# Kernel optimization log

Hardware: AMD Instinct MI355X
Metric: run time of the kernel (lower is better)

The kernel has to match this reference:

```python
import jax, jax.numpy as jnp
import numpy as np

N_NODES = 100000
N_EDGES = 3200000
N_GRAPHS = 1024

def _lin(x, W, b):
    return x @ W.T + b

def _gine(x, src, dst, edge_attr, W, b, n_nodes):
    # message = relu(x_j + e); aggregate sum at dst; out = Linear(x + aggr)  (eps=0)
    msg = jax.nn.relu(x[src] + edge_attr)
    aggr = jax.ops.segment_sum(msg, dst, num_segments=n_nodes)
    return _lin(x + aggr, W, b)

def setup_inputs() -> dict:
    key = jax.random.key(0)
    ks = jax.random.split(key, 20)
    D_NODE, D_EDGE, H, OUT = 12, 4, 15, 2
    inp = {
        "x": jax.random.normal(ks[0], (N_NODES, D_NODE), dtype=jnp.float32),
        "edge_index": jax.random.randint(ks[1], (2, N_EDGES), 0, N_NODES, dtype=jnp.int64),
        "edge_attr": jax.random.normal(ks[2], (N_EDGES, D_EDGE), dtype=jnp.float32),
        "batch": jnp.sort(jax.random.randint(ks[3], (N_NODES,), 0, N_GRAPHS, dtype=jnp.int64)),
        # edge converters
        "Wec1": jax.random.normal(ks[4], (D_NODE, D_EDGE), dtype=jnp.float32) * 0.3,
        "bec1": jnp.zeros((D_NODE,), jnp.float32),
        "Wec2": jax.random.normal(ks[5], (H, D_NODE), dtype=jnp.float32) * 0.2,
        "bec2": jnp.zeros((H,), jnp.float32),
        # GINE layer linears
        "Wl0": jax.random.normal(ks[6], (H, D_NODE), dtype=jnp.float32) * 0.2,
        "bl0": jnp.zeros((H,), jnp.float32),
        "Wl1": jax.random.normal(ks[7], (H, H), dtype=jnp.float32) * 0.2,
        "bl1": jnp.zeros((H,), jnp.float32),
        "Wl2": jax.random.normal(ks[8], (H, H), dtype=jnp.float32) * 0.2,
        "bl2": jnp.zeros((H,), jnp.float32),
        # output head
        "Wo1": jax.random.normal(ks[9], (H, H), dtype=jnp.float32) * 0.2,
        "bo1": jnp.zeros((H,), jnp.float32),
        "Wo2": jax.random.normal(ks[10], (OUT, H), dtype=jnp.float32) * 0.2,
        "bo2": jnp.zeros((OUT,), jnp.float32),
    }
    return inp

def reference(x, edge_index, edge_attr, batch,
              Wec1, bec1, Wec2, bec2,
              Wl0, bl0, Wl1, bl1, Wl2, bl2,
              Wo1, bo1, Wo2, bo2):
    src, dst = edge_index[0], edge_index[1]
    n = x.shape[0]
    ea = _lin(edge_attr, Wec1, bec1)                 # [E, 12]
    h = jax.nn.elu(_gine(x, src, dst, ea, Wl0, bl0, n))   # [N, 15]
    ea2 = _lin(ea, Wec2, bec2)                       # [E, 15]
    h = jax.nn.elu(_gine(h, src, dst, ea2, Wl1, bl1, n))
    h = jax.nn.elu(_gine(h, src, dst, ea2, Wl2, bl2, n))
    pooled = jax.ops.segment_sum(h, batch, num_segments=N_GRAPHS)  # [G, 15]
    out = _lin(pooled, Wo1, bo1)
    # dropout(p=0.1) is identity in eval mode
    out = _lin(out, Wo2, bo2)                        # [G, 2]
    return out
```

## Files before the change

kernel.cpp:

```cpp
#include <hip/hip_runtime.h>
#include <hip/hip_fp16.h>
#include <math.h>

#define D_NODE 12
#define HS     16
#define BSH    7
#define BSZ    128
#define CHUNK  8192
#define HALF   4096
#define MAXNB  1024

__device__ __forceinline__ int wave_iscan(int v, int lane) {
#pragma unroll
    for (int d = 1; d < 64; d <<= 1) {
        int u = __shfl_up(v, d, 64);
        if (lane >= d) v += u;
    }
    return v;
}

__device__ __forceinline__ uint2 pack4(float4 a) {
    __half2 lo = __floats2half2_rn(a.x, a.y);
    __half2 hi = __floats2half2_rn(a.z, a.w);
    uint2 r;
    r.x = *reinterpret_cast<unsigned*>(&lo);
    r.y = *reinterpret_cast<unsigned*>(&hi);
    return r;
}

__device__ __forceinline__ float4 unpack4(unsigned ux, unsigned uy) {
    __half2 lo = *reinterpret_cast<__half2*>(&ux);
    __half2 hi = *reinterpret_cast<__half2*>(&uy);
    float2 f0 = __half22float2(lo), f1 = __half22float2(hi);
    return make_float4(f0.x, f0.y, f1.x, f1.y);
}

__global__ __launch_bounds__(256) void k_xcvt(
    const float* __restrict__ x, long long nn, __half* __restrict__ xp)
{
    long long idx = (long long)blockIdx.x * 256 + threadIdx.x;
    if (idx >= nn * HS) return;
    long long n = idx >> 4;
    int l = (int)(idx & 15);
    xp[idx] = __float2half_rn((l < D_NODE) ? x[n * D_NODE + l] : 0.f);
}

__global__ __launch_bounds__(1024) void k_p1(
    const int* __restrict__ ei, long long ne, int NB, int* __restrict__ M)
{
    __shared__ int cnt[MAXNB];
    int t = threadIdx.x;
    for (int k = t; k < NB; k += 1024) cnt[k] = 0;
    __syncthreads();
    long long beg = (long long)blockIdx.x * CHUNK;
    long long end = beg + CHUNK; if (end > ne) end = ne;
    for (long long e = beg + t; e < end; e += 1024)
        atomicAdd(&cnt[ei[ne + e] >> BSH], 1);
    __syncthreads();
    int* row = M + (long long)blockIdx.x * NB;
    for (int k = t; k < NB; k += 1024) row[k] = cnt[k];
}

__global__ __launch_bounds__(256) void k_colscan(
    int* __restrict__ M, int nblk, int NB, int* __restrict__ tot)
{
    __shared__ int wsum[4];
    int k = blockIdx.x;
    int t = threadIdx.x;
    int lane = t & 63, wv = t >> 6;
    int v[4]; int s = 0;
#pragma unroll
    for (int j = 0; j < 4; ++j) {
        int b = t * 4 + j;
        v[j] = (b < nblk) ? M[(long long)b * NB + k] : 0;
        s += v[j];
    }
    int inc = wave_iscan(s, lane);
    if (lane == 63) wsum[wv] = inc;
    __syncthreads();
    int base = inc - s;
#pragma unroll
    for (int j = 0; j < 4; ++j) { if (j < wv) base += wsum[j]; }
#pragma unroll
    for (int j = 0; j < 4; ++j) {
        int b = t * 4 + j;
        if (b < nblk) { M[(long long)b * NB + k] = base; base += v[j]; }
    }
    if (t == 255) tot[k] = base;
}

__global__ __launch_bounds__(1024) void k_bb(
    const int* __restrict__ tot, int NB, int* __restrict__ bb)
{
    __shared__ int wsum[16];
    int t = threadIdx.x;
    int lane = t & 63, wv = t >> 6;
    int c = (t < NB) ? tot[t] : 0;
    int inc = wave_iscan(c, lane);
    if (lane == 63) wsum[wv] = inc;
    __syncthreads();
    if (t < 16) {
        int s2 = wsum[t];
#pragma unroll
        for (int d = 1; d < 16; d <<= 1) {
            int u = __shfl_up(s2, d, 64);
            if (t >= d) s2 += u;
        }
        wsum[t] = s2;
    }
    __syncthreads();
    int base = (wv == 0) ? 0 : wsum[wv - 1];
    int incl = base + inc;
    if (t < NB) bb[t] = incl - c;
    if (t == NB - 1) bb[NB] = incl;
}

__global__ __launch_bounds__(1024) void k_p2(
    const int* __restrict__ ei, long long ne, const float4* __restrict__ attr,
    const int* __restrict__ M, const int* __restrict__ bb, int NB,
    unsigned* __restrict__ sp1, uint2* __restrict__ sattr1)
{
    __shared__ int lcnt[MAXNB];
    __shared__ int excl[MAXNB];
    __shared__ int gb[MAXNB];
    __shared__ int wsum[16];
    __shared__ unsigned sp_st[HALF];
    __shared__ uint2   sat_st[HALF];
    __shared__ int     gd_st[HALF];
    int t = threadIdx.x;
    int lane = t & 63, wv = t >> 6;
    const int* row = M + (long long)blockIdx.x * NB;
    gb[t]   = (t < NB) ? (bb[t] + row[t]) : 0;
    lcnt[t] = 0;
    __syncthreads();
    long long beg = (long long)blockIdx.x * CHUNK;
    long long end = beg + CHUNK; if (end > ne) end = ne;
    int nloc = (int)(end - beg);
    unsigned pk8[8]; uint2 a8[8]; int k8[8], r8[8];
#pragma unroll
    for (int j = 0; j < 8; ++j) {
        long long e = beg + t + (long long)j * 1024;
        if (e < end) {
            int s = ei[e];
            int d = ei[ne + e];
            a8[j] = pack4(attr[e]);
            int k = d >> BSH;
            k8[j] = k;
            pk8[j] = (unsigned)s | ((unsigned)(d & (BSZ - 1)) << 20);
            r8[j] = atomicAdd(&lcnt[k], 1);
        } else k8[j] = -1;
    }
    __syncthreads();
    int c = lcnt[t];
    int inc = wave_iscan(c, lane);
    if (lane == 63) wsum[wv] = inc;
    __syncthreads();
    if (t < 16) {
        int s2 = wsum[t];
#pragma unroll
        for (int d = 1; d < 16; d <<= 1) {
            int u = __shfl_up(s2, d, 64);
            if (t >= d) s2 += u;
        }
        wsum[t] = s2;
    }
    __syncthreads();
    excl[t] = inc - c + ((wv == 0) ? 0 : wsum[wv - 1]);
    __syncthreads();
    int idx8[8];
#pragma unroll
    for (int j = 0; j < 8; ++j)
        idx8[j] = (k8[j] >= 0) ? (excl[k8[j]] + r8[j]) : -1;
#pragma unroll
    for (int q = 0; q < 2; ++q) {
        int lo = q * HALF;
#pragma unroll
        for (int j = 0; j < 8; ++j) {
            int idx = idx8[j] - lo;
            if (idx8[j] >= 0 && idx >= 0 && idx < HALF) {
                sp_st[idx]  = pk8[j];
                sat_st[idx] = a8[j];
                gd_st[idx]  = gb[k8[j]] + r8[j];
            }
        }
        __syncthreads();
        for (int p = t; p < HALF; p += 1024) {
            int gp = lo + p;
            if (gp < nloc) {
                int gd = gd_st[p];
                sp1[gd]    = sp_st[p];
                sattr1[gd] = sat_st[p];
            }
        }
        __syncthreads();
    }
}

__global__ __launch_bounds__(1024) void k_p3(
    const unsigned* __restrict__ sp1, const uint2* __restrict__ sattr1,
    const int* __restrict__ bb, int NB, long long nn,
    unsigned* __restrict__ sp2, uint2* __restrict__ sattr2, int* __restrict__ off)
{
    __shared__ int cnt[BSZ];
    __shared__ int stage[BSZ];
    __shared__ int wsum0;
    int k = blockIdx.x, t = threadIdx.x;
    int lane = t & 63, wv = t >> 6;
    int beg = bb[k], end = bb[k + 1];
    if (t < BSZ) cnt[t] = 0;
    __syncthreads();
    for (int e = beg + t; e < end; e += 1024)
        atomicAdd(&cnt[sp1[e] >> 20], 1);
    __syncthreads();
    if (t < BSZ) {
        int c = cnt[t];
        int inc = wave_iscan(c, lane);
        stage[t] = inc;
        if (lane == 63 && wv == 0) wsum0 = inc;
    }
    __syncthreads();
    if (t < BSZ) {
        int c = cnt[t];
        int incl = stage[t] + ((wv == 1) ? wsum0 : 0);
        int excl = beg + incl - c;
        long long n = (long long)k * BSZ + t;
        if (n < nn) off[n] = excl;
        cnt[t] = excl;
    }
    if (k == NB - 1 && t == 0) off[nn] = end;
    __syncthreads();
    for (int e = beg + t; e < end; e += 1024) {
        unsigned pk = sp1[e];
        int ld = pk >> 20;
        int p = atomicAdd(&cnt[ld], 1);
        sp2[p] = pk & 0xFFFFF;
        sattr2[p] = sattr1[e];
    }
}

__global__ __launch_bounds__(256) void k_layer0(
    const __half* __restrict__ xp, long long nn, const int* __restrict__ off,
    const unsigned* __restrict__ sp2, const uint2* __restrict__ sattr2,
    const float* __restrict__ Wec1, const float* __restrict__ bec1,
    const float* __restrict__ Wl, const float* __restrict__ bl,
    __half* __restrict__ hout)
{
    __shared__ float sW1[64], sb1[16], sWl[16 * 17], sbl[16];
    int t = threadIdx.x;
    if (t < 64)  sW1[t] = (t < 48) ? Wec1[t] : 0.f;
    if (t < 16)  sb1[t] = (t < 12) ? bec1[t] : 0.f;
    { int i = t >> 4, j = t & 15;
      sWl[i * 17 + j] = (i < 15 && j < 12) ? Wl[i * 12 + j] : 0.f; }
    if (t < 16)  sbl[t] = (t < 15) ? bl[t] : 0.f;
    __syncthreads();
    int wv = t >> 6;
    int lane = t & 63;
    int l = lane & 15;
    int slot = lane >> 4;
    long long n = (long long)blockIdx.x * 4 + wv;
    if (n >= nn) return;
    int beg = off[n], end = off[n + 1];
    float w0 = sW1[l*4+0], w1 = sW1[l*4+1], w2 = sW1[l*4+2], w3 = sW1[l*4+3];
    float b1 = sb1[l];
    float xn = __half2float(xp[(n << 4) + l]);
    float acc = 0.f;
#pragma unroll 2
    for (int e0 = beg; e0 < end; e0 += 4) {
        int e = e0 + slot;
        unsigned sp = sp2[e] & 0xFFFFF;
        uint2 at = sattr2[e];
        float4 a = unpack4(at.x, at.y);
        float xs = __half2float(xp[((long long)sp << 4) + l]);
        float ea = b1 + w0 * a.x + w1 * a.y + w2 * a.z + w3 * a.w;
        float m = fmaxf(xs + ea, 0.f);
        acc += (e < end) ? m : 0.f;
    }
    acc += __shfl_xor(acc, 16, 64);
    acc += __shfl_xor(acc, 32, 64);
    float v = xn + acc;
    float r = sbl[l];
#pragma unroll
    for (int j = 0; j < 12; ++j) {
        float vj = __shfl(v, j, 16);
        r += vj * sWl[l * 17 + j];
    }
    float o = r > 0.f ? r : expm1f(r);
    if (slot == 0)
        hout[(n << 4) + l] = __float2half_rn((l < 15) ? o : 0.f);
}

template<bool POOL, bool STORE>
__global__ __launch_bounds__(256) void k_layerK(
    const __half* __restrict__ h, long long nn, const int* __restrict__ off,
    const unsigned* __restrict__ sp2, const uint2* __restrict__ sattr2,
    const float* __restrict__ Wec1, const float* __restrict__ bec1,
    const float* __restrict__ Wec2, const float* __restrict__ bec2,
    const float* __restrict__ Wl, const float* __restrict__ bl,
    __half* __restrict__ hout, const int* __restrict__ batch, float* __restrict__ pooled)
{
    __shared__ float sW12[64], sb12[16], sWl[16 * 17], sbl[16];
    int t = threadIdx.x;
    if (t < 64) {
        int i = t >> 2, kk = t & 3;
        float a = 0.f;
        if (i < 15) {
#pragma unroll
            for (int j = 0; j < 12; ++j) a += Wec2[i*12+j] * Wec1[j*4+kk];
        }
        sW12[t] = a;
    }
    if (t < 16) {
        float a = 0.f;
        if (t < 15) {
            a = bec2[t];
#pragma unroll
            for (int j = 0; j < 12; ++j) a += Wec2[t*12+j] * bec1[j];
        }
        sb12[t] = a;
    }
    { int i = t >> 4, j = t & 15;
      sWl[i * 17 + j] = (i < 15 && j < 15) ? Wl[i * 15 + j] : 0.f; }
    if (t < 16) sbl[t] = (t < 15) ? bl[t] : 0.f;
    __syncthreads();
    int wv = t >> 6;
    int lane = t & 63;
    int l = lane & 15;
    int slot = lane >> 4;
    long long n = (long long)blockIdx.x * 4 + wv;
    if (n >= nn) return;
    int beg = off[n], end = off[n + 1];
    float w0 = sW12[l*4+0], w1 = sW12[l*4+1], w2 = sW12[l*4+2], w3 = sW12[l*4+3];
    float b12 = sb12[l];
    float hn = __half2float(h[(n << 4) + l]);
    float acc = 0.f;
#pragma unroll 2
    for (int e0 = beg; e0 < end; e0 += 4) {
        int e = e0 + slot;
        unsigned sp = sp2[e] & 0xFFFFF;
        uint2 at = sattr2[e];
        float4 a = unpack4(at.x, at.y);
        float hs = __half2float(h[((long long)sp << 4) + l]);
        float e2 = b12 + w0 * a.x + w1 * a.y + w2 * a.z + w3 * a.w;
        float m = fmaxf(hs + e2, 0.f);
        acc += (e < end) ? m : 0.f;
    }
    acc += __shfl_xor(acc, 16, 64);
    acc += __shfl_xor(acc, 32, 64);
    float v = hn + acc;
    float r = sbl[l];
#pragma unroll
    for (int j = 0; j < 15; ++j) {
        float vj = __shfl(v, j, 16);
        r += vj * sWl[l * 17 + j];
    }
    float o = r > 0.f ? r : expm1f(r);
    if (slot == 0) {
        if (STORE) hout[(n << 4) + l] = __float2half_rn((l < 15) ? o : 0.f);
        if (POOL && l < 15) atomicAdd(&pooled[(long long)batch[n] * HS + l], o);
    }
}

__global__ __launch_bounds__(256) void k_head(
    const float* __restrict__ pooled, long long ng,
    const float* __restrict__ Wo1, const float* __restrict__ bo1,
    const float* __restrict__ Wo2, const float* __restrict__ bo2,
    float* __restrict__ out)
{
    long long g = (long long)blockIdx.x * 256 + threadIdx.x;
    if (g >= ng) return;
    float p[15], m[15];
#pragma unroll
    for (int j = 0; j < 15; ++j) p[j] = pooled[g * HS + j];
#pragma unroll
    for (int i = 0; i < 15; ++i) {
        float acc = bo1[i];
#pragma unroll
        for (int j = 0; j < 15; ++j) acc += p[j] * Wo1[i * 15 + j];
        m[i] = acc;
    }
#pragma unroll
    for (int i = 0; i < 2; ++i) {
        float acc = bo2[i];
#pragma unroll
        for (int j = 0; j < 15; ++j) acc += m[j] * Wo2[i * 15 + j];
        out[g * 2 + i] = acc;
    }
}

extern "C" void kernel_launch(void* const* d_in, const int* in_sizes, int n_in,
                              void* d_out, int out_size, void* d_ws, size_t ws_size,
                              hipStream_t stream)
{
    const float* x    = (const float*)d_in[0];
    const int*   ei   = (const int*)d_in[1];
    const float* attr = (const float*)d_in[2];
    const int*   batch= (const int*)d_in[3];
    const float* Wec1 = (const float*)d_in[4];
    const float* bec1 = (const float*)d_in[5];
    const float* Wec2 = (const float*)d_in[6];
    const float* bec2 = (const float*)d_in[7];
    const float* Wl0  = (const float*)d_in[8];
    const float* bl0  = (const float*)d_in[9];
    const float* Wl1  = (const float*)d_in[10];
    const float* bl1  = (const float*)d_in[11];
    const float* Wl2  = (const float*)d_in[12];
    const float* bl2  = (const float*)d_in[13];
    const float* Wo1  = (const float*)d_in[14];
    const float* bo1  = (const float*)d_in[15];
    const float* Wo2  = (const float*)d_in[16];
    const float* bo2  = (const float*)d_in[17];

    const long long nn = in_sizes[0] / D_NODE;
    const long long ne = in_sizes[1] / 2;
    const long long ng = out_size / 2;

    const int NB   = (int)((nn + BSZ - 1) >> BSH);
    const int nblk = (int)((ne + CHUNK - 1) / CHUNK);
    const long long nep = ne + 8;

    char* w = (char*)d_ws;
    uint2*    sattr1 = (uint2*)w;                 w += (size_t)nep * sizeof(uint2);
    unsigned* sp1    = (unsigned*)w;              w += (size_t)nep * sizeof(unsigned);
    uint2*    sattr2 = (uint2*)w;                 w += (size_t)nep * sizeof(uint2);
    unsigned* sp2    = (unsigned*)w;              w += (size_t)nep * sizeof(unsigned);
    int*      M      = (int*)w;                   w += (size_t)nblk * NB * sizeof(int);
    int*      tot    = (int*)w;                   w += (size_t)NB * sizeof(int);
    int*      bb     = (int*)w;                   w += ((size_t)NB + 1) * sizeof(int);
    int*      off    = (int*)w;                   w += ((size_t)nn + 1) * sizeof(int);
    w = (char*)(((uintptr_t)w + 15) & ~(uintptr_t)15);
    __half*   xp     = (__half*)w;                w += (size_t)nn * HS * sizeof(__half);
    __half*   hA     = (__half*)sattr1;
    __half*   hB     = hA + (size_t)nn * HS;
    float*    pooled = (float*)(hB + (size_t)nn * HS);
    float*    out    = (float*)d_out;

    k_xcvt<<<(int)((nn * HS + 255) / 256), 256, 0, stream>>>(x, nn, xp);

    k_p1<<<nblk, 1024, 0, stream>>>(ei, ne, NB, M);
    k_colscan<<<NB, 256, 0, stream>>>(M, nblk, NB, tot);
    k_bb<<<1, 1024, 0, stream>>>(tot, NB, bb);
    k_p2<<<nblk, 1024, 0, stream>>>(ei, ne, (const float4*)attr, M, bb, NB, sp1, sattr1);
    k_p3<<<NB, 1024, 0, stream>>>(sp1, sattr1, bb, NB, nn, sp2, sattr2, off);

    const int lblk = (int)((nn + 3) / 4);
    k_layer0<<<lblk, 256, 0, stream>>>(xp, nn, off, sp2, sattr2, Wec1, bec1, Wl0, bl0, hA);
    k_layerK<false, true><<<lblk, 256, 0, stream>>>(hA, nn, off, sp2, sattr2,
        Wec1, bec1, Wec2, bec2, Wl1, bl1, hB, nullptr, nullptr);
    hipMemsetAsync(pooled, 0, (size_t)ng * HS * sizeof(float), stream);
    k_layerK<true, false><<<lblk, 256, 0, stream>>>(hB, nn, off, sp2, sattr2,
        Wec1, bec1, Wec2, bec2, Wl2, bl2, nullptr, batch, pooled);

    k_head<<<(int)((ng + 255) / 256), 256, 0, stream>>>(pooled, ng, Wo1, bo1, Wo2, bo2, out);
}
```

Measured before the change: 324.8 us.

## Remap GINE layer lanes to process 16 edges per wave with 4-wide feature vectors

Changes the thread mapping in the layer kernels so each lane handles 4 feature channels (8-byte half loads) and a wave covers 16 edges per iteration instead of 4. This raises edge-level parallelism per wave and cuts redundant per-edge index and attribute loads, which were repeated 16 times per edge before. The cost is more registers, a longer shuffle reduction and a reworked matvec via cross-lane shuffles. Padding of the sorted edge arrays grows to 16 and the tail of sp2 is zeroed so out-of-range lanes read a valid row.

Measured after the change: 294.8 us. -9.2%, faster.

```diff
diff --git a/kernel.cpp b/kernel.cpp
--- a/kernel.cpp
+++ b/kernel.cpp
@@ -253,40 +253,61 @@
       sWl[i * 17 + j] = (i < 15 && j < 12) ? Wl[i * 12 + j] : 0.f; }
     if (t < 16)  sbl[t] = (t < 15) ? bl[t] : 0.f;
     __syncthreads();
-    int wv = t >> 6;
-    int lane = t & 63;
-    int l = lane & 15;
-    int slot = lane >> 4;
+    int lane = t & 63, wv = t >> 6;
+    int d4 = lane & 3;
+    int slot = lane >> 2;
     long long n = (long long)blockIdx.x * 4 + wv;
     if (n >= nn) return;
     int beg = off[n], end = off[n + 1];
-    float w0 = sW1[l*4+0], w1 = sW1[l*4+1], w2 = sW1[l*4+2], w3 = sW1[l*4+3];
-    float b1 = sb1[l];
-    float xn = __half2float(xp[(n << 4) + l]);
-    float acc = 0.f;
-#pragma unroll 2
-    for (int e0 = beg; e0 < end; e0 += 4) {
+    float w1r[4][4], b1r[4];
+#pragma unroll
+    for (int j = 0; j < 4; ++j) {
+        b1r[j] = sb1[d4 * 4 + j];
+#pragma unroll
+        for (int k = 0; k < 4; ++k) w1r[j][k] = sW1[(d4 * 4 + j) * 4 + k];
+    }
+    float acc[4] = {0.f, 0.f, 0.f, 0.f};
+    for (int e0 = beg; e0 < end; e0 += 16) {
         int e = e0 + slot;
         unsigned sp = sp2[e] & 0xFFFFF;
         uint2 at = sattr2[e];
         float4 a = unpack4(at.x, at.y);
-        float xs = __half2float(xp[((long long)sp << 4) + l]);
-        float ea = b1 + w0 * a.x + w1 * a.y + w2 * a.z + w3 * a.w;
-        float m = fmaxf(xs + ea, 0.f);
-        acc += (e < end) ? m : 0.f;
-    }
-    acc += __shfl_xor(acc, 16, 64);
-    acc += __shfl_xor(acc, 32, 64);
-    float v = xn + acc;
+        uint2 hv = *reinterpret_cast<const uint2*>(
+            reinterpret_cast<const char*>(xp) + ((size_t)sp << 5) + (d4 << 3));
+        float4 hf = unpack4(hv.x, hv.y);
+        float hvf[4] = {hf.x, hf.y, hf.z, hf.w};
+        bool val = (e < end);
+#pragma unroll
+        for (int j = 0; j < 4; ++j) {
+            float ea = b1r[j] + w1r[j][0]*a.x + w1r[j][1]*a.y + w1r[j][2]*a.z + w1r[j][3]*a.w;
+            float m = fmaxf(hvf[j] + ea, 0.f);
+            acc[j] += val ? m : 0.f;
+        }
+    }
+#pragma unroll
+    for (int j = 0; j < 4; ++j) {
+        acc[j] += __shfl_xor(acc[j], 4, 64);
+        acc[j] += __shfl_xor(acc[j], 8, 64);
+        acc[j] += __shfl_xor(acc[j], 16, 64);
+        acc[j] += __shfl_xor(acc[j], 32, 64);
+    }
+    uint2 hnv = *reinterpret_cast<const uint2*>(
+        reinterpret_cast<const char*>(xp) + ((size_t)n << 5) + (d4 << 3));
+    float4 hnf = unpack4(hnv.x, hnv.y);
+    float v4[4] = {hnf.x + acc[0], hnf.y + acc[1], hnf.z + acc[2], hnf.w + acc[3]};
+    int l = lane & 15;
     float r = sbl[l];
 #pragma unroll
-    for (int j = 0; j < 12; ++j) {
-        float vj = __shfl(v, j, 16);
-        r += vj * sWl[l * 17 + j];
+    for (int a2 = 0; a2 < 4; ++a2) {
+#pragma unroll
+        for (int b2 = 0; b2 < 4; ++b2) {
+            float vv = __shfl(v4[b2], a2, 64);
+            r += vv * sWl[l * 17 + a2 * 4 + b2];
+        }
     }
     float o = r > 0.f ? r : expm1f(r);
-    if (slot == 0)
-        hout[(n << 4) + l] = __float2half_rn((l < 15) ? o : 0.f);
+    if (lane < 16)
+        hout[(n << 4) + lane] = __float2half_rn((lane < 15) ? o : 0.f);
 }
 
 template<bool POOL, bool STORE>
@@ -322,41 +343,62 @@
       sWl[i * 17 + j] = (i < 15 && j < 15) ? Wl[i * 15 + j] : 0.f; }
     if (t < 16) sbl[t] = (t < 15) ? bl[t] : 0.f;
     __syncthreads();
-    int wv = t >> 6;
-    int lane = t & 63;
-    int l = lane & 15;
-    int slot = lane >> 4;
+    int lane = t & 63, wv = t >> 6;
+    int d4 = lane & 3;
+    int slot = lane >> 2;
     long long n = (long long)blockIdx.x * 4 + wv;
     if (n >= nn) return;
     int beg = off[n], end = off[n + 1];
-    float w0 = sW12[l*4+0], w1 = sW12[l*4+1], w2 = sW12[l*4+2], w3 = sW12[l*4+3];
-    float b12 = sb12[l];
-    float hn = __half2float(h[(n << 4) + l]);
-    float acc = 0.f;
-#pragma unroll 2
-    for (int e0 = beg; e0 < end; e0 += 4) {
+    float w12r[4][4], b12r[4];
+#pragma unroll
+    for (int j = 0; j < 4; ++j) {
+        b12r[j] = sb12[d4 * 4 + j];
+#pragma unroll
+        for (int k = 0; k < 4; ++k) w12r[j][k] = sW12[(d4 * 4 + j) * 4 + k];
+    }
+    float acc[4] = {0.f, 0.f, 0.f, 0.f};
+    for (int e0 = beg; e0 < end; e0 += 16) {
         int e = e0 + slot;
         unsigned sp = sp2[e] & 0xFFFFF;
         uint2 at = sattr2[e];
         float4 a = unpack4(at.x, at.y);
-        float hs = __half2float(h[((long long)sp << 4) + l]);
-        float e2 = b12 + w0 * a.x + w1 * a.y + w2 * a.z + w3 * a.w;
-        float m = fmaxf(hs + e2, 0.f);
-        acc += (e < end) ? m : 0.f;
-    }
-    acc += __shfl_xor(acc, 16, 64);
-    acc += __shfl_xor(acc, 32, 64);
-    float v = hn + acc;
+        uint2 hv = *reinterpret_cast<const uint2*>(
+            reinterpret_cast<const char*>(h) + ((size_t)sp << 5) + (d4 << 3));
+        float4 hf = unpack4(hv.x, hv.y);
+        float hvf[4] = {hf.x, hf.y, hf.z, hf.w};
+        bool val = (e < end);
+#pragma unroll
+        for (int j = 0; j < 4; ++j) {
+            float e2 = b12r[j] + w12r[j][0]*a.x + w12r[j][1]*a.y + w12r[j][2]*a.z + w12r[j][3]*a.w;
+            float m = fmaxf(hvf[j] + e2, 0.f);
+            acc[j] += val ? m : 0.f;
+        }
+    }
+#pragma unroll
+    for (int j = 0; j < 4; ++j) {
+        acc[j] += __shfl_xor(acc[j], 4, 64);
+        acc[j] += __shfl_xor(acc[j], 8, 64);
+        acc[j] += __shfl_xor(acc[j], 16, 64);
+        acc[j] += __shfl_xor(acc[j], 32, 64);
+    }
+    uint2 hnv = *reinterpret_cast<const uint2*>(
+        reinterpret_cast<const char*>(h) + ((size_t)n << 5) + (d4 << 3));
+    float4 hnf = unpack4(hnv.x, hnv.y);
+    float v4[4] = {hnf.x + acc[0], hnf.y + acc[1], hnf.z + acc[2], hnf.w + acc[3]};
+    int l = lane & 15;
     float r = sbl[l];
 #pragma unroll
-    for (int j = 0; j < 15; ++j) {
-        float vj = __shfl(v, j, 16);
-        r += vj * sWl[l * 17 + j];
+    for (int a2 = 0; a2 < 4; ++a2) {
+#pragma unroll
+        for (int b2 = 0; b2 < 4; ++b2) {
+            float vv = __shfl(v4[b2], a2, 64);
+            r += vv * sWl[l * 17 + a2 * 4 + b2];
+        }
     }
     float o = r > 0.f ? r : expm1f(r);
-    if (slot == 0) {
-        if (STORE) hout[(n << 4) + l] = __float2half_rn((l < 15) ? o : 0.f);
-        if (POOL && l < 15) atomicAdd(&pooled[(long long)batch[n] * HS + l], o);
+    if (lane < 16) {
+        if (STORE) hout[(n << 4) + lane] = __float2half_rn((lane < 15) ? o : 0.f);
+        if (POOL && lane < 15) atomicAdd(&pooled[(long long)batch[n] * HS + lane], o);
     }
 }
 
@@ -416,7 +458,7 @@
 
     const int NB   = (int)((nn + BSZ - 1) >> BSH);
     const int nblk = (int)((ne + CHUNK - 1) / CHUNK);
-    const long long nep = ne + 8;
+    const long long nep = ne + 16;
 
     char* w = (char*)d_ws;
     uint2*    sattr1 = (uint2*)w;                 w += (size_t)nep * sizeof(uint2);
@@ -441,6 +483,7 @@
     k_bb<<<1, 1024, 0, stream>>>(tot, NB, bb);
     k_p2<<<nblk, 1024, 0, stream>>>(ei, ne, (const float4*)attr, M, bb, NB, sp1, sattr1);
     k_p3<<<NB, 1024, 0, stream>>>(sp1, sattr1, bb, NB, nn, sp2, sattr2, off);
+    hipMemsetAsync(sp2 + ne, 0, 16 * sizeof(unsigned), stream);
 
     const int lblk = (int)((nn + 3) / 4);
     k_layer0<<<lblk, 256, 0, stream>>>(xp, nn, off, sp2, sattr2, Wec1, bec1, Wl0, bl0, hA);
```
